# Kernel optimization log

Measured on AMD Instinct MI355X. Metric: run time of the kernel, lower is better.

The kernel has to match this reference:

```python
import jax, jax.numpy as jnp
import numpy as np

N, E, H, NIN, DD = 10000, 160000, 128, 128, 256
SCALE = 30.0
EPS = 1e-5

def _ln(x, g, b):
    mu = jnp.mean(x, axis=-1, keepdims=True)
    var = jnp.mean((x - mu) ** 2, axis=-1, keepdims=True)
    return (x - mu) * jax.lax.rsqrt(var + EPS) * g + b

def _gelu(x):
    return jax.nn.gelu(x, approximate=False)  # torch nn.GELU default (erf)

def setup_inputs() -> dict:
    key = jax.random.key(0)
    ks = jax.random.split(key, 16)
    def w(k, i, o):
        return jax.random.normal(k, (i, o), jnp.float32) * (1.0 / np.sqrt(i))
    return {
        "h_V": jax.random.normal(ks[0], (N, H), jnp.float32),
        "h_E": jax.random.normal(ks[1], (E, H + NIN), jnp.float32),
        "edge_idx": jax.random.randint(ks[2], (2, E), 0, N, jnp.int32),
        # message MLP: (H+NIN)->H, H->H
        "m_w0": w(ks[3], H + NIN, H), "m_b0": jnp.zeros((H,), jnp.float32),
        "m_w1": w(ks[4], H, H),       "m_b1": jnp.zeros((H,), jnp.float32),
        # dense MLP: H->DD, DD->DD, final DD->H
        "d_w0": w(ks[5], H, DD),  "d_b0": jnp.zeros((DD,), jnp.float32),
        "d_w1": w(ks[6], DD, DD), "d_b1": jnp.zeros((DD,), jnp.float32),
        "d_w2": w(ks[7], DD, H),  "d_b2": jnp.zeros((H,), jnp.float32),
        # LayerNorm params
        "g1": jnp.ones((H,), jnp.float32), "be1": jnp.zeros((H,), jnp.float32),
        "g2": jnp.ones((H,), jnp.float32), "be2": jnp.zeros((H,), jnp.float32),
    }

def reference(h_V, h_E, edge_idx, m_w0, m_b0, m_w1, m_b1,
              d_w0, d_b0, d_w1, d_b1, d_w2, d_b2, g1, be1, g2, be2):
    src_idx = edge_idx[0]
    # message MLP over edges (dropout = identity at inference)
    h = _gelu(h_E @ m_w0 + m_b0)
    h_message = _gelu(h @ m_w1 + m_b1)          # [E, H]
    # scatter-sum aggregate edges -> nodes
    dh = jax.ops.segment_sum(h_message, src_idx, num_segments=N) / SCALE
    h_V = _ln(h_V + dh, g1, be1)
    # dense MLP over nodes
    d = _gelu(h_V @ d_w0 + d_b0)
    d = _gelu(d @ d_w1 + d_b1)
    dh = d @ d_w2 + d_b2
    return _ln(h_V + dh, g2, be2)
```

## Files before the change

### kernel.cpp

```cpp
#include <hip/hip_runtime.h>
#include <hip/hip_bf16.h>


typedef __attribute__((ext_vector_type(8))) short bf16x8;
typedef __attribute__((ext_vector_type(4))) float f32x4;

__device__ __forceinline__ unsigned short f2bf(float f) {
  union { float f; unsigned u; } v; v.f = f;
  return (unsigned short)((v.u + 0x7fffu + ((v.u >> 16) & 1u)) >> 16);
}
__device__ __forceinline__ unsigned pk2bf(float a, float b) {
  __hip_bfloat162 h = __float22bfloat162_rn(make_float2(a, b));
  union { __hip_bfloat162 h; unsigned u; } v; v.h = h;
  return v.u;
}
__device__ __forceinline__ float bf2f(unsigned s) {
  union { unsigned u; float f; } v; v.u = s << 16;
  return v.f;
}
__device__ __forceinline__ float gelu_f(float x) {
  float u = x * 0.70710678118654752f;
  float au = fabsf(u);
  float t = __builtin_amdgcn_rcpf(1.0f + 0.3275911f * au);
  float poly = ((((1.061405429f * t - 1.453152027f) * t + 1.421413741f) * t -
                 0.284496736f) * t + 0.254829592f) * t;
  float e = __expf(-au * au);
  float erfu = copysignf(1.0f - poly * e, u);
  return 0.5f * x * (1.0f + erfu);
}

__global__ void k_pack(const float* __restrict__ mw0, const float* __restrict__ mw1,
                       const float* __restrict__ dw0, const float* __restrict__ dw1,
                       const float* __restrict__ dw2,
                       unsigned short* __restrict__ pw0, unsigned short* __restrict__ pw1,
                       unsigned short* __restrict__ pd0, unsigned short* __restrict__ pd1,
                       unsigned short* __restrict__ pd2,
                       int* __restrict__ counts, int Nn) {
  int g = blockIdx.x, lane = threadIdx.x;
  int z = g * 64 + lane;
  if (z < Nn) counts[z] = 0;
  const float* src; unsigned short* dst; int K, N, WC, base;
  if (g < 64)       { src = mw0; dst = pw0; K = 256; N = 128; WC = 128; base = 0; }
  else if (g < 96)  { src = mw1; dst = pw1; K = 128; N = 128; WC = 128; base = 64; }
  else if (g < 160) { src = dw0; dst = pd0; K = 128; N = 256; WC = 64; base = 96; }
  else if (g < 288) { src = dw1; dst = pd1; K = 256; N = 256; WC = 64; base = 160; }
  else              { src = dw2; dst = pd2; K = 256; N = 128; WC = 32; base = 288; }
  int lg = g - base;
  int KS = K >> 5, CTKS = (WC >> 4) * KS;
  int w = lg / CTKS, rem = lg % CTKS, ct = rem / KS, ks = rem % KS;
  int col = w * WC + ct * 16 + (lane & 15);
  int k0 = ks * 32 + (lane >> 4) * 8;
  unsigned short o[8];
#pragma unroll
  for (int j = 0; j < 8; ++j) o[j] = f2bf(src[(size_t)(k0 + j) * N + col]);
  uint4 u;
  u.x = (unsigned)o[0] | ((unsigned)o[1] << 16);
  u.y = (unsigned)o[2] | ((unsigned)o[3] << 16);
  u.z = (unsigned)o[4] | ((unsigned)o[5] << 16);
  u.w = (unsigned)o[6] | ((unsigned)o[7] << 16);
  *(uint4*)(dst + (size_t)(lg * 64 + lane) * 8) = u;
}

__global__ void k_hist(const int* __restrict__ eidx, int* __restrict__ counts, int E) {
  int e = blockIdx.x * 256 + threadIdx.x;
  if (e < E) atomicAdd(&counts[eidx[e]], 1);
}

__global__ __launch_bounds__(1024) void k_scan(const int* __restrict__ counts,
                                               int* __restrict__ row_start,
                                               int* __restrict__ cursor, int Nn) {
  __shared__ int sm[1024];
  int t = threadIdx.x;
  int chunk = (Nn + 1023) / 1024;
  int lo = t * chunk, hi = lo + chunk;
  if (hi > Nn) hi = Nn;
  int s = 0;
  for (int i = lo; i < hi; ++i) s += counts[i];
  sm[t] = s;
  __syncthreads();
  for (int o = 1; o < 1024; o <<= 1) {
    int u = (t >= o) ? sm[t - o] : 0;
    __syncthreads();
    sm[t] += u;
    __syncthreads();
  }
  int run = sm[t] - s;
  for (int i = lo; i < hi; ++i) {
    row_start[i] = run; cursor[i] = run; run += counts[i];
  }
  if (t == 1023) row_start[Nn] = sm[1023];
}

__global__ void k_scatter(const int* __restrict__ eidx, int* __restrict__ cursor,
                          int* __restrict__ eorder, int E) {
  int e = blockIdx.x * 256 + threadIdx.x;
  if (e < E) {
    int pos = atomicAdd(&cursor[eidx[e]], 1);
    eorder[pos] = e;
  }
}

__global__ __launch_bounds__(256) void k_edge(
    const float* __restrict__ hE, const unsigned short* __restrict__ pw0,
    const unsigned short* __restrict__ pw1, const float* __restrict__ b0,
    const float* __restrict__ b1, unsigned short* __restrict__ hmsg, int E) {
  __shared__ __align__(16) char lds[4 * 4096];
  const int tid = threadIdx.x;
  const int wid = tid >> 6, lane = tid & 63;
  const int l15 = lane & 15, lhi = lane >> 4;
  char* Hw = lds + wid * 4096;

  const int wt = blockIdx.x * 4 + wid;
  const int row0w = wt * 16;
  if (row0w >= E) return;

  float bb0[8], bb1[8];
#pragma unroll
  for (int ct = 0; ct < 8; ++ct) {
    bb0[ct] = b0[ct * 16 + l15];
    bb1[ct] = b1[ct * 16 + l15];
  }

  int rowA = row0w + l15; rowA = rowA < E ? rowA : E - 1;
  const float* ap = hE + (size_t)rowA * 256 + lhi * 8;
  f32x4 av[16];
#pragma unroll
  for (int ks = 0; ks < 8; ++ks) {
    av[2 * ks]     = *(const f32x4*)(ap + ks * 32);
    av[2 * ks + 1] = *(const f32x4*)(ap + ks * 32 + 4);
  }

  f32x4 acc[8];
#pragma unroll
  for (int ct = 0; ct < 8; ++ct) acc[ct] = 0.f;
#pragma unroll
  for (int ks = 0; ks < 8; ++ks) {
    union { unsigned u[4]; bf16x8 v; } pk;
    pk.u[0] = pk2bf(av[2 * ks][0], av[2 * ks][1]);
    pk.u[1] = pk2bf(av[2 * ks][2], av[2 * ks][3]);
    pk.u[2] = pk2bf(av[2 * ks + 1][0], av[2 * ks + 1][1]);
    pk.u[3] = pk2bf(av[2 * ks + 1][2], av[2 * ks + 1][3]);
#pragma unroll
    for (int ct = 0; ct < 8; ++ct) {
      uint4 bv = ((const uint4*)pw0)[(size_t)(ct * 8 + ks) * 64 + lane];
      bf16x8 b = *(bf16x8*)&bv;
      acc[ct] = __builtin_amdgcn_mfma_f32_16x16x32_bf16(pk.v, b, acc[ct], 0, 0, 0);
    }
  }
#pragma unroll
  for (int ct = 0; ct < 8; ++ct)
#pragma unroll
    for (int j = 0; j < 4; ++j) {
      int r = lhi * 4 + j, col = ct * 16 + l15;
      *(unsigned short*)(Hw + r * 256 + ((col * 2) ^ ((r & 7) << 4))) =
          f2bf(gelu_f(acc[ct][j] + bb0[ct]));
    }

  f32x4 acc2[8];
#pragma unroll
  for (int ct = 0; ct < 8; ++ct) acc2[ct] = 0.f;
#pragma unroll
  for (int ks = 0; ks < 4; ++ks) {
    bf16x8 a = *(bf16x8*)(Hw + l15 * 256 + ((ks * 64 + lhi * 16) ^ ((l15 & 7) << 4)));
#pragma unroll
    for (int ct = 0; ct < 8; ++ct) {
      uint4 bv = ((const uint4*)pw1)[(size_t)(ct * 4 + ks) * 64 + lane];
      bf16x8 b = *(bf16x8*)&bv;
      acc2[ct] = __builtin_amdgcn_mfma_f32_16x16x32_bf16(a, b, acc2[ct], 0, 0, 0);
    }
  }
#pragma unroll
  for (int ct = 0; ct < 8; ++ct)
#pragma unroll
    for (int j = 0; j < 4; ++j) {
      int r = lhi * 4 + j, col = ct * 16 + l15;
      *(unsigned short*)(Hw + r * 256 + ((col * 2) ^ ((r & 7) << 4))) =
          f2bf(gelu_f(acc2[ct][j] + bb1[ct]));
    }
  {
    int r = lane >> 2, cb = (lane & 3) * 64;
    int grow = row0w + r;
    if (grow < E) {
      uint4* dst = (uint4*)(hmsg + (size_t)grow * 128) + (lane & 3) * 4;
#pragma unroll
      for (int q = 0; q < 4; ++q)
        dst[q] = *(uint4*)(Hw + r * 256 + ((cb + q * 16) ^ ((r & 7) << 4)));
    }
  }
}

__global__ __launch_bounds__(256) void k_aggln(
    const unsigned* __restrict__ hmsg, const float2* __restrict__ hV,
    const int* __restrict__ row_start, const int* __restrict__ eorder,
    const float* __restrict__ g1, const float* __restrict__ be1,
    float2* __restrict__ hv1f, unsigned* __restrict__ hv1b, int Nn) {
  int wid = threadIdx.x >> 6, lane = threadIdx.x & 63;
  int node = blockIdx.x * 4 + wid;
  if (node >= Nn) return;
  int s = row_start[node], e = row_start[node + 1];
  float s0 = 0.f, s1 = 0.f;
  int i = s;
  for (; i + 3 < e; i += 4) {
    int e0 = eorder[i], e1 = eorder[i + 1], e2 = eorder[i + 2], e3 = eorder[i + 3];
    unsigned v0 = hmsg[(size_t)e0 * 64 + lane];
    unsigned v1 = hmsg[(size_t)e1 * 64 + lane];
    unsigned v2 = hmsg[(size_t)e2 * 64 + lane];
    unsigned v3 = hmsg[(size_t)e3 * 64 + lane];
    s0 += bf2f(v0 & 0xffffu) + bf2f(v1 & 0xffffu) + bf2f(v2 & 0xffffu) + bf2f(v3 & 0xffffu);
    s1 += bf2f(v0 >> 16) + bf2f(v1 >> 16) + bf2f(v2 >> 16) + bf2f(v3 >> 16);
  }
  for (; i < e; ++i) {
    unsigned v = hmsg[(size_t)eorder[i] * 64 + lane];
    s0 += bf2f(v & 0xffffu);
    s1 += bf2f(v >> 16);
  }
  float2 hv = hV[(size_t)node * 64 + lane];
  float x0 = hv.x + s0 * (1.f / 30.f);
  float x1 = hv.y + s1 * (1.f / 30.f);
  float sum = x0 + x1, sq = x0 * x0 + x1 * x1;
#pragma unroll
  for (int off = 32; off > 0; off >>= 1) {
    sum += __shfl_xor(sum, off);
    sq += __shfl_xor(sq, off);
  }
  float mu = sum * (1.f / 128.f);
  float var = sq * (1.f / 128.f) - mu * mu;
  float rs = rsqrtf(var + 1e-5f);
  int c = lane * 2;
  float y0 = (x0 - mu) * rs * g1[c] + be1[c];
  float y1 = (x1 - mu) * rs * g1[c + 1] + be1[c + 1];
  hv1f[(size_t)node * 64 + lane] = make_float2(y0, y1);
  hv1b[(size_t)node * 64 + lane] = (unsigned)f2bf(y0) | ((unsigned)f2bf(y1) << 16);
}

__global__ __launch_bounds__(256, 4) void k_node(
    const unsigned short* __restrict__ xb, const unsigned short* __restrict__ pd0,
    const unsigned short* __restrict__ pd1, const unsigned short* __restrict__ pd2,
    const float* __restrict__ db0, const float* __restrict__ db1,
    const float* __restrict__ db2, const float* __restrict__ hv1f,
    const float* __restrict__ g2, const float* __restrict__ be2,
    float* __restrict__ out, int Nn) {
  __shared__ __align__(16) char lds[8192 + 16384 + 16384];
  char* A0 = lds;
  char* D0 = lds + 8192;
  char* D1 = lds + 8192 + 16384;
  float* Y = (float*)D0;
  const int tid = threadIdx.x, wid = tid >> 6, lane = tid & 63;
  const int l15 = lane & 15, lhi = lane >> 4;
  const int row0 = blockIdx.x * 32;

  {
    int idx = tid;
    int r = idx >> 3, c = idx & 7;
    uint4 v = make_uint4(0u, 0u, 0u, 0u);
    if (row0 + r < Nn) v = ((const uint4*)xb)[(size_t)(row0 + r) * 16 + c * 2];
    *(uint4*)(A0 + r * 256 + ((c * 32) ^ ((r & 7) << 4))) = v;
    uint4 v2 = make_uint4(0u, 0u, 0u, 0u);
    if (row0 + r < Nn) v2 = ((const uint4*)xb)[(size_t)(row0 + r) * 16 + c * 2 + 1];
    *(uint4*)(A0 + r * 256 + (((c * 32) + 16) ^ ((r & 7) << 4))) = v2;
  }
  __syncthreads();

  {
    f32x4 acc[2][4];
#pragma unroll
    for (int mt = 0; mt < 2; ++mt)
#pragma unroll
      for (int ct = 0; ct < 4; ++ct) acc[mt][ct] = 0.f;
#pragma unroll
    for (int ks = 0; ks < 4; ++ks) {
      bf16x8 a[2];
#pragma unroll
      for (int mt = 0; mt < 2; ++mt) {
        int row = mt * 16 + l15;
        a[mt] = *(bf16x8*)(A0 + row * 256 + ((ks * 64 + lhi * 16) ^ ((row & 7) << 4)));
      }
#pragma unroll
      for (int ct = 0; ct < 4; ++ct) {
        uint4 bv = ((const uint4*)pd0)[(size_t)(wid * 16 + ct * 4 + ks) * 64 + lane];
        bf16x8 b = *(bf16x8*)&bv;
#pragma unroll
        for (int mt = 0; mt < 2; ++mt)
          acc[mt][ct] = __builtin_amdgcn_mfma_f32_16x16x32_bf16(a[mt], b, acc[mt][ct], 0, 0, 0);
      }
    }
#pragma unroll
    for (int ct = 0; ct < 4; ++ct) {
      float bb = db0[wid * 64 + ct * 16 + l15];
      int col = wid * 64 + ct * 16 + l15;
#pragma unroll
      for (int mt = 0; mt < 2; ++mt)
#pragma unroll
        for (int j = 0; j < 4; ++j) {
          int r = mt * 16 + lhi * 4 + j;
          *(unsigned short*)(D0 + r * 512 + ((col * 2) ^ ((r & 7) << 4))) =
              f2bf(gelu_f(acc[mt][ct][j] + bb));
        }
    }
  }
  __syncthreads();

  {
    f32x4 acc[2][4];
#pragma unroll
    for (int mt = 0; mt < 2; ++mt)
#pragma unroll
      for (int ct = 0; ct < 4; ++ct) acc[mt][ct] = 0.f;
#pragma unroll
    for (int ks = 0; ks < 8; ++ks) {
      bf16x8 a[2];
#pragma unroll
      for (int mt = 0; mt < 2; ++mt) {
        int row = mt * 16 + l15;
        a[mt] = *(bf16x8*)(D0 + row * 512 + ((ks * 64 + lhi * 16) ^ ((row & 7) << 4)));
      }
#pragma unroll
      for (int ct = 0; ct < 4; ++ct) {
        uint4 bv = ((const uint4*)pd1)[(size_t)(wid * 32 + ct * 8 + ks) * 64 + lane];
        bf16x8 b = *(bf16x8*)&bv;
#pragma unroll
        for (int mt = 0; mt < 2; ++mt)
          acc[mt][ct] = __builtin_amdgcn_mfma_f32_16x16x32_bf16(a[mt], b, acc[mt][ct], 0, 0, 0);
      }
    }
#pragma unroll
    for (int ct = 0; ct < 4; ++ct) {
      float bb = db1[wid * 64 + ct * 16 + l15];
      int col = wid * 64 + ct * 16 + l15;
#pragma unroll
      for (int mt = 0; mt < 2; ++mt)
#pragma unroll
        for (int j = 0; j < 4; ++j) {
          int r = mt * 16 + lhi * 4 + j;
          *(unsigned short*)(D1 + r * 512 + ((col * 2) ^ ((r & 7) << 4))) =
              f2bf(gelu_f(acc[mt][ct][j] + bb));
        }
    }
  }
  __syncthreads();

  {
    f32x4 acc[2][2];
#pragma unroll
    for (int mt = 0; mt < 2; ++mt)
#pragma unroll
      for (int ct = 0; ct < 2; ++ct) acc[mt][ct] = 0.f;
#pragma unroll
    for (int ks = 0; ks < 8; ++ks) {
      bf16x8 a[2];
#pragma unroll
      for (int mt = 0; mt < 2; ++mt) {
        int row = mt * 16 + l15;
        a[mt] = *(bf16x8*)(D1 + row * 512 + ((ks * 64 + lhi * 16) ^ ((row & 7) << 4)));
      }
#pragma unroll
      for (int ct = 0; ct < 2; ++ct) {
        uint4 bv = ((const uint4*)pd2)[(size_t)(wid * 16 + ct * 8 + ks) * 64 + lane];
        bf16x8 b = *(bf16x8*)&bv;
#pragma unroll
        for (int mt = 0; mt < 2; ++mt)
          acc[mt][ct] = __builtin_amdgcn_mfma_f32_16x16x32_bf16(a[mt], b, acc[mt][ct], 0, 0, 0);
      }
    }
    __syncthreads();
#pragma unroll
    for (int ct = 0; ct < 2; ++ct) {
      float bb = db2[wid * 32 + ct * 16 + l15];
      int col = wid * 32 + ct * 16 + l15;
#pragma unroll
      for (int mt = 0; mt < 2; ++mt)
#pragma unroll
        for (int j = 0; j < 4; ++j) {
          int r = mt * 16 + lhi * 4 + j;
          int grow = row0 + r;
          float res = (grow < Nn) ? hv1f[(size_t)grow * 128 + col] : 0.f;
          Y[r * 128 + col] = acc[mt][ct][j] + bb + res;
        }
    }
  }
  __syncthreads();

  float g2a = g2[lane * 2], g2b = g2[lane * 2 + 1];
  float ba = be2[lane * 2], bbx = be2[lane * 2 + 1];
  for (int ii = 0; ii < 8; ++ii) {
    int r = wid * 8 + ii;
    int grow = row0 + r;
    if (grow >= Nn) continue;
    float2 xy = *(float2*)&Y[r * 128 + lane * 2];
    float sum = xy.x + xy.y, sq = xy.x * xy.x + xy.y * xy.y;
#pragma unroll
    for (int off = 32; off > 0; off >>= 1) {
      sum += __shfl_xor(sum, off);
      sq += __shfl_xor(sq, off);
    }
    float mu = sum * (1.f / 128.f);
    float var = sq * (1.f / 128.f) - mu * mu;
    float rs = rsqrtf(var + 1e-5f);
    float y0 = (xy.x - mu) * rs * g2a + ba;
    float y1 = (xy.y - mu) * rs * g2b + bbx;
    *(float2*)&out[(size_t)grow * 128 + lane * 2] = make_float2(y0, y1);
  }
}

extern "C" void kernel_launch(void* const* d_in, const int* in_sizes, int n_in,
                              void* d_out, int out_size, void* d_ws, size_t ws_size,
                              hipStream_t stream) {
  const float* hV  = (const float*)d_in[0];
  const float* hE  = (const float*)d_in[1];
  const int* eidx  = (const int*)d_in[2];
  const float* mw0 = (const float*)d_in[3];
  const float* mb0 = (const float*)d_in[4];
  const float* mw1 = (const float*)d_in[5];
  const float* mb1 = (const float*)d_in[6];
  const float* dw0 = (const float*)d_in[7];
  const float* db0 = (const float*)d_in[8];
  const float* dw1 = (const float*)d_in[9];
  const float* db1 = (const float*)d_in[10];
  const float* dw2 = (const float*)d_in[11];
  const float* db2 = (const float*)d_in[12];
  const float* g1  = (const float*)d_in[13];
  const float* be1 = (const float*)d_in[14];
  const float* g2  = (const float*)d_in[15];
  const float* be2 = (const float*)d_in[16];
  const int Nn = in_sizes[0] / 128;
  const int E  = in_sizes[1] / 256;

  char* ws = (char*)d_ws;
  size_t off = 0;
  auto alloc = [&](size_t bytes) -> char* {
    off = (off + 255) & ~(size_t)255;
    char* p = ws + off;
    off += bytes;
    return p;
  };
  unsigned short* hmsg = (unsigned short*)alloc((size_t)E * 128 * 2);
  float* hv1f          = (float*)alloc((size_t)Nn * 128 * 4);
  unsigned short* hv1b = (unsigned short*)alloc((size_t)Nn * 128 * 2);
  unsigned short* pw0  = (unsigned short*)alloc(32768 * 2);
  unsigned short* pw1  = (unsigned short*)alloc(16384 * 2);
  unsigned short* pd0  = (unsigned short*)alloc(32768 * 2);
  unsigned short* pd1  = (unsigned short*)alloc(65536 * 2);
  unsigned short* pd2  = (unsigned short*)alloc(32768 * 2);
  int* counts    = (int*)alloc((size_t)Nn * 4);
  int* row_start = (int*)alloc((size_t)(Nn + 1) * 4);
  int* cursor    = (int*)alloc((size_t)Nn * 4);
  int* eorder    = (int*)alloc((size_t)E * 4);

  k_pack<<<352, 64, 0, stream>>>(mw0, mw1, dw0, dw1, dw2, pw0, pw1, pd0, pd1, pd2,
                                 counts, Nn);
  k_hist<<<(E + 255) / 256, 256, 0, stream>>>(eidx, counts, E);
  k_scan<<<1, 1024, 0, stream>>>(counts, row_start, cursor, Nn);
  k_scatter<<<(E + 255) / 256, 256, 0, stream>>>(eidx, cursor, eorder, E);
  k_edge<<<(E + 63) / 64, 256, 0, stream>>>(hE, pw0, pw1, mb0, mb1, hmsg, E);
  k_aggln<<<(Nn + 3) / 4, 256, 0, stream>>>((const unsigned*)hmsg, (const float2*)hV,
                                            row_start, eorder, g1, be1,
                                            (float2*)hv1f, (unsigned*)hv1b, Nn);
  const int nt = (Nn + 31) / 32;
  k_node<<<nt, 256, 0, stream>>>(hv1b, pd0, pd1, pd2, db0, db1, db2,
                                 hv1f, g2, be2, (float*)d_out, Nn);
}
```

Before: 151.1 us.

## Make edge MLP persistent with LDS-resident weights and prefetched next tile

The edge-MLP kernel becomes a persistent grid of 256 blocks of 512 threads. Each block stages both packed weight matrices (96 KB) into LDS once, then loops over 16-row edge tiles, loading the next tile's fp32 inputs into registers while the current tile's MFMAs run. This is meant to remove repeated global/L2 weight fetches per tile and hide input-load latency. In exchange it uses 128 KB of LDS per block, which limits occupancy to one block per CU and adds register pressure from the prefetch buffers.

New measurement: 199.1 us. +31.7%, slower.

```diff
diff --git a/kernel.cpp b/kernel.cpp
--- a/kernel.cpp
+++ b/kernel.cpp
@@ -100,91 +100,121 @@
   }
 }
 
-__global__ __launch_bounds__(256) void k_edge(
+__global__ void k_edge(
     const float* __restrict__ hE, const unsigned short* __restrict__ pw0,
     const unsigned short* __restrict__ pw1, const float* __restrict__ b0,
     const float* __restrict__ b1, unsigned short* __restrict__ hmsg, int E) {
-  __shared__ __align__(16) char lds[4 * 4096];
+  __shared__ __align__(16) char lds[131072];
   const int tid = threadIdx.x;
   const int wid = tid >> 6, lane = tid & 63;
   const int l15 = lane & 15, lhi = lane >> 4;
-  char* Hw = lds + wid * 4096;
-
-  const int wt = blockIdx.x * 4 + wid;
-  const int row0w = wt * 16;
-  if (row0w >= E) return;
-
+  char* Hw = lds + 98304 + wid * 4096;
+
+  {
+    const uint4* s0 = (const uint4*)pw0;
+    const uint4* s1 = (const uint4*)pw1;
+    uint4* d = (uint4*)lds;
+#pragma unroll
+    for (int i = 0; i < 12; ++i) {
+      int idx = i * 512 + tid;
+      d[idx] = (idx < 4096) ? s0[idx] : s1[idx - 4096];
+    }
+  }
   float bb0[8], bb1[8];
 #pragma unroll
   for (int ct = 0; ct < 8; ++ct) {
     bb0[ct] = b0[ct * 16 + l15];
     bb1[ct] = b1[ct * 16 + l15];
   }
-
-  int rowA = row0w + l15; rowA = rowA < E ? rowA : E - 1;
-  const float* ap = hE + (size_t)rowA * 256 + lhi * 8;
+  __syncthreads();
+
+  const int TILES = (E + 15) >> 4;
+  const int WSLOTS = gridDim.x * 8;
+  int t = blockIdx.x * 8 + wid;
+  if (t >= TILES) return;
+
   f32x4 av[16];
-#pragma unroll
-  for (int ks = 0; ks < 8; ++ks) {
-    av[2 * ks]     = *(const f32x4*)(ap + ks * 32);
-    av[2 * ks + 1] = *(const f32x4*)(ap + ks * 32 + 4);
-  }
-
-  f32x4 acc[8];
-#pragma unroll
-  for (int ct = 0; ct < 8; ++ct) acc[ct] = 0.f;
-#pragma unroll
-  for (int ks = 0; ks < 8; ++ks) {
-    union { unsigned u[4]; bf16x8 v; } pk;
-    pk.u[0] = pk2bf(av[2 * ks][0], av[2 * ks][1]);
-    pk.u[1] = pk2bf(av[2 * ks][2], av[2 * ks][3]);
-    pk.u[2] = pk2bf(av[2 * ks + 1][0], av[2 * ks + 1][1]);
-    pk.u[3] = pk2bf(av[2 * ks + 1][2], av[2 * ks + 1][3]);
-#pragma unroll
-    for (int ct = 0; ct < 8; ++ct) {
-      uint4 bv = ((const uint4*)pw0)[(size_t)(ct * 8 + ks) * 64 + lane];
-      bf16x8 b = *(bf16x8*)&bv;
-      acc[ct] = __builtin_amdgcn_mfma_f32_16x16x32_bf16(pk.v, b, acc[ct], 0, 0, 0);
-    }
-  }
-#pragma unroll
-  for (int ct = 0; ct < 8; ++ct)
-#pragma unroll
-    for (int j = 0; j < 4; ++j) {
-      int r = lhi * 4 + j, col = ct * 16 + l15;
-      *(unsigned short*)(Hw + r * 256 + ((col * 2) ^ ((r & 7) << 4))) =
-          f2bf(gelu_f(acc[ct][j] + bb0[ct]));
-    }
-
-  f32x4 acc2[8];
-#pragma unroll
-  for (int ct = 0; ct < 8; ++ct) acc2[ct] = 0.f;
-#pragma unroll
-  for (int ks = 0; ks < 4; ++ks) {
-    bf16x8 a = *(bf16x8*)(Hw + l15 * 256 + ((ks * 64 + lhi * 16) ^ ((l15 & 7) << 4)));
-#pragma unroll
-    for (int ct = 0; ct < 8; ++ct) {
-      uint4 bv = ((const uint4*)pw1)[(size_t)(ct * 4 + ks) * 64 + lane];
-      bf16x8 b = *(bf16x8*)&bv;
-      acc2[ct] = __builtin_amdgcn_mfma_f32_16x16x32_bf16(a, b, acc2[ct], 0, 0, 0);
-    }
-  }
-#pragma unroll
-  for (int ct = 0; ct < 8; ++ct)
-#pragma unroll
-    for (int j = 0; j < 4; ++j) {
-      int r = lhi * 4 + j, col = ct * 16 + l15;
-      *(unsigned short*)(Hw + r * 256 + ((col * 2) ^ ((r & 7) << 4))) =
-          f2bf(gelu_f(acc2[ct][j] + bb1[ct]));
-    }
-  {
-    int r = lane >> 2, cb = (lane & 3) * 64;
-    int grow = row0w + r;
-    if (grow < E) {
-      uint4* dst = (uint4*)(hmsg + (size_t)grow * 128) + (lane & 3) * 4;
-#pragma unroll
-      for (int q = 0; q < 4; ++q)
-        dst[q] = *(uint4*)(Hw + r * 256 + ((cb + q * 16) ^ ((r & 7) << 4)));
+  {
+    int rowA = t * 16 + l15; rowA = rowA < E ? rowA : E - 1;
+    const float* ap = hE + (size_t)rowA * 256 + lhi * 8;
+#pragma unroll
+    for (int ks = 0; ks < 8; ++ks) {
+      av[2 * ks]     = *(const f32x4*)(ap + ks * 32);
+      av[2 * ks + 1] = *(const f32x4*)(ap + ks * 32 + 4);
+    }
+  }
+
+  for (; t < TILES; t += WSLOTS) {
+    const int tn = t + WSLOTS;
+    bf16x8 af[8];
+#pragma unroll
+    for (int ks = 0; ks < 8; ++ks) {
+      union { unsigned u[4]; bf16x8 v; } pk;
+      pk.u[0] = pk2bf(av[2 * ks][0], av[2 * ks][1]);
+      pk.u[1] = pk2bf(av[2 * ks][2], av[2 * ks][3]);
+      pk.u[2] = pk2bf(av[2 * ks + 1][0], av[2 * ks + 1][1]);
+      pk.u[3] = pk2bf(av[2 * ks + 1][2], av[2 * ks + 1][3]);
+      af[ks] = pk.v;
+    }
+    if (tn < TILES) {
+      int rowA = tn * 16 + l15; rowA = rowA < E ? rowA : E - 1;
+      const float* ap = hE + (size_t)rowA * 256 + lhi * 8;
+#pragma unroll
+      for (int ks = 0; ks < 8; ++ks) {
+        av[2 * ks]     = *(const f32x4*)(ap + ks * 32);
+        av[2 * ks + 1] = *(const f32x4*)(ap + ks * 32 + 4);
+      }
+    }
+
+    f32x4 acc[8];
+#pragma unroll
+    for (int ct = 0; ct < 8; ++ct) acc[ct] = 0.f;
+#pragma unroll
+    for (int ks = 0; ks < 8; ++ks)
+#pragma unroll
+      for (int ct = 0; ct < 8; ++ct) {
+        bf16x8 b = *(bf16x8*)(lds + (ct * 8 + ks) * 1024 + lane * 16);
+        acc[ct] = __builtin_amdgcn_mfma_f32_16x16x32_bf16(af[ks], b, acc[ct], 0, 0, 0);
+      }
+#pragma unroll
+    for (int ct = 0; ct < 8; ++ct)
+#pragma unroll
+      for (int j = 0; j < 4; ++j) {
+        int r = lhi * 4 + j, col = ct * 16 + l15;
+        *(unsigned short*)(Hw + r * 256 + ((col * 2) ^ ((r & 7) << 4))) =
+            f2bf(gelu_f(acc[ct][j] + bb0[ct]));
+      }
+
+    f32x4 acc2[8];
+#pragma unroll
+    for (int ct = 0; ct < 8; ++ct) acc2[ct] = 0.f;
+#pragma unroll
+    for (int ks = 0; ks < 4; ++ks) {
+      bf16x8 a = *(bf16x8*)(Hw + l15 * 256 + ((ks * 64 + lhi * 16) ^ ((l15 & 7) << 4)));
+#pragma unroll
+      for (int ct = 0; ct < 8; ++ct) {
+        bf16x8 b = *(bf16x8*)(lds + 65536 + (ct * 4 + ks) * 1024 + lane * 16);
+        acc2[ct] = __builtin_amdgcn_mfma_f32_16x16x32_bf16(a, b, acc2[ct], 0, 0, 0);
+      }
+    }
+#pragma unroll
+    for (int ct = 0; ct < 8; ++ct)
+#pragma unroll
+      for (int j = 0; j < 4; ++j) {
+        int r = lhi * 4 + j, col = ct * 16 + l15;
+        *(unsigned short*)(Hw + r * 256 + ((col * 2) ^ ((r & 7) << 4))) =
+            f2bf(gelu_f(acc2[ct][j] + bb1[ct]));
+      }
+    {
+      int r = lane >> 2;
+      int grow = t * 16 + r;
+      if (grow < E) {
+        uint4* dst = (uint4*)(hmsg + (size_t)grow * 128) + (lane & 3) * 4;
+        int cb = (lane & 3) * 64;
+#pragma unroll
+        for (int q = 0; q < 4; ++q)
+          dst[q] = *(uint4*)(Hw + r * 256 + ((cb + q * 16) ^ ((r & 7) << 4)));
+      }
     }
   }
 }
@@ -451,7 +481,7 @@
   k_hist<<<(E + 255) / 256, 256, 0, stream>>>(eidx, counts, E);
   k_scan<<<1, 1024, 0, stream>>>(counts, row_start, cursor, Nn);
   k_scatter<<<(E + 255) / 256, 256, 0, stream>>>(eidx, cursor, eorder, E);
-  k_edge<<<(E + 63) / 64, 256, 0, stream>>>(hE, pw0, pw1, mb0, mb1, hmsg, E);
+  k_edge<<<256, 512, 0, stream>>>(hE, pw0, pw1, mb0, mb1, hmsg, E);
   k_aggln<<<(Nn + 3) / 4, 256, 0, stream>>>((const unsigned*)hmsg, (const float2*)hV,
                                             row_start, eorder, g1, be1,
                                             (float2*)hv1f, (unsigned*)hv1b, Nn);
```
